# Kernel optimization log

Hardware: AMD Instinct MI355X
Metric: run time of the kernel (lower is better)

The kernel has to match this reference:

```python
import jax, jax.numpy as jnp
import numpy as np

B, T, V, D = 16, 200, 25, 128
N_Q, N_E = 4, 1024
BETA, ALPHA, SLOPE, LN_EPS = 0.25, 0.1, 0.2, 1e-5

def _ring_adjacency(v):
    A = np.zeros((v, v), dtype=np.float32)
    for i in range(v):
        A[i, (i + 1) % v] = 1.0
        A[i, (i - 1) % v] = 1.0
    A = A + np.eye(v, dtype=np.float32)  # A + I, as in module
    d_inv_sqrt = 1.0 / np.sqrt(A.sum(1))
    return (d_inv_sqrt[:, None] * A) * d_inv_sqrt[None, :]

def setup_inputs() -> dict:
    key = jax.random.key(0)
    k_z, k_e, k_w = jax.random.split(key, 3)
    z = jax.random.normal(k_z, (B, T, V, D), dtype=jnp.float32)
    # xavier_uniform for each [n_e, e_dim] codebook
    lim = float(np.sqrt(6.0 / (N_E + D)))
    emb = jax.random.uniform(k_e, (N_Q, N_E, D), dtype=jnp.float32, minval=-lim, maxval=lim)
    wlim = float(np.sqrt(1.0 / D))
    gcn_w = jax.random.uniform(k_w, (D, D), dtype=jnp.float32, minval=-wlim, maxval=wlim)
    return {
        "z": z,
        "emb": emb,
        "A_norm": jnp.asarray(_ring_adjacency(V)),
        "gcn_w": gcn_w,
        "gcn_b": jnp.zeros((D,), jnp.float32),
        "ln_scale": jnp.ones((D,), jnp.float32),
        "ln_bias": jnp.zeros((D,), jnp.float32),
    }

def _gcn_refine(residual, A_norm, gcn_w, gcn_b, ln_scale, ln_bias):
    # residual: [N, V, d]
    neigh = jnp.einsum('vw,nwd->nvd', A_norm, residual)
    neigh = neigh @ gcn_w.T + gcn_b                      # nn.Linear
    neigh = jnp.where(neigh >= 0, neigh, SLOPE * neigh)  # LeakyReLU(0.2)
    mu = neigh.mean(-1, keepdims=True)
    var = ((neigh - mu) ** 2).mean(-1, keepdims=True)
    neigh = (neigh - mu) / jnp.sqrt(var + LN_EPS) * ln_scale + ln_bias
    return residual + ALPHA * neigh

def reference(z, emb, A_norm, gcn_w, gcn_b, ln_scale, ln_bias):
    b, t, v, d = z.shape
    n_q = emb.shape[0]
    zf = z.reshape(b * t, v, d)
    residual = zf
    cum = jnp.zeros_like(zf)
    losses, idxs = [], []
    for k in range(n_q):
        refined = _gcn_refine(residual, A_norm, gcn_w, gcn_b, ln_scale, ln_bias)
        W = emb[k]                               # [n_e, d]
        flat = refined.reshape(-1, d)            # [N*V, d]
        dist = ((flat ** 2).sum(1, keepdims=True)
                - 2.0 * flat @ W.T
                + (W ** 2).sum(1)[None, :])
        idx = jnp.argmin(dist, axis=1)           # [N*V]
        q = W[idx].reshape(b * t, v, d)          # == one_hot @ W
        # commit and codebook terms are identical squared errors -> (1+beta)*mse
        diff = q - jax.lax.stop_gradient(residual)
        losses.append((1.0 + BETA) * (diff ** 2).mean(-1))
        cum = cum + q
        residual = residual - q
        idxs.append(idx.reshape(b * t, v))
    zq = zf + jax.lax.stop_gradient(cum - zf)    # straight-through
    total_loss = jnp.stack(losses, 0).mean()
    indices = jnp.stack(idxs, -1).reshape(b, t, v, n_q)
    return zq.reshape(b, t, v, d), total_loss, indices
```

## Files before the change

kernel.cpp:

```cpp
#include <hip/hip_runtime.h>

#define ZQ_N    10240000
#define IDX_OFF 10240001
#define FLT_BIG 3.402823466e38f

typedef _Float16 f16x8 __attribute__((ext_vector_type(8)));
typedef float    f32x4 __attribute__((ext_vector_type(4)));

__global__ __launch_bounds__(256) void k_wsq(const float* __restrict__ emb,
                                             float* __restrict__ wsq,
                                             float* __restrict__ loss_part) {
    int t = threadIdx.x;
    int g = blockIdx.x * 256 + t;
    if (g < 1024) loss_part[g] = 0.f;
    int row = blockIdx.x * 64 + (t >> 2);
    int seg = t & 3;
    const float4* p = (const float4*)(emb + row * 128 + seg * 32);
    float a = 0.f;
#pragma unroll
    for (int i = 0; i < 8; i++) {
        float4 w = p[i];
        a = fmaf(w.x, w.x, a); a = fmaf(w.y, w.y, a);
        a = fmaf(w.z, w.z, a); a = fmaf(w.w, w.w, a);
    }
    a += __shfl_xor(a, 1);
    a += __shfl_xor(a, 2);
    if (seg == 0) wsq[row] = a;
}

__global__ __launch_bounds__(256) void k_wsplit(const float* __restrict__ emb,
        _Float16* __restrict__ wh, _Float16* __restrict__ wl,
        const float* __restrict__ gw,
        _Float16* __restrict__ gh, _Float16* __restrict__ gl) {
    int c = blockIdx.x * 256 + threadIdx.x;
    int q   = c >> 14;
    int col = (c >> 4) & 1023;
    int k8  = (c & 15) * 8;
    const float* srcp = emb + q * 131072 + col * 128 + k8;
    float4 a = *(const float4*)(srcp);
    float4 b = *(const float4*)(srcp + 4);
    float vv[8] = {a.x, a.y, a.z, a.w, b.x, b.y, b.z, b.w};
    union { _Float16 h[8]; uint4 u4; } ph, pl;
#pragma unroll
    for (int j = 0; j < 8; j++) {
        float v = vv[j] * 1024.f;
        _Float16 h = (_Float16)v;
        float r1 = v - (float)h;
        ph.h[j] = h; pl.h[j] = (_Float16)r1;
    }
    int w  = col >> 7, p = (col >> 4) & 7, lm = col & 15;
    int ks = k8 >> 5, quad = (k8 >> 3) & 3;
    int off = ((w * 8 + p) * 4 + ks) * 512 + (quad * 16 + lm) * 8;
    *(uint4*)(wh + q * 131072 + off) = ph.u4;
    *(uint4*)(wl + q * 131072 + off) = pl.u4;

    if (c < 16384) {
        float v = gw[c] * 1024.f;
        _Float16 h = (_Float16)v;
        float r1 = v - (float)h;
        gh[c] = h; gl[c] = (_Float16)r1;
    }
}

__global__ __launch_bounds__(256) void k_refine(const float* __restrict__ zbase,
        const float* __restrict__ emb, const float* __restrict__ idx_f, int stage,
        float* __restrict__ refined, float* __restrict__ s_out,
        const float* __restrict__ An,
        const _Float16* __restrict__ gh, const _Float16* __restrict__ gl,
        const float* __restrict__ gb, const float* __restrict__ lsc,
        const float* __restrict__ lbi) {
    __shared__ __align__(16) float Rn[25 * 128];
    __shared__ __align__(16) unsigned char nbuf[2 * 32 * 136 * 2];
    __shared__ float Al[625];
    __shared__ int cds[75];
    _Float16* nh = (_Float16*)nbuf;
    _Float16* nl = (_Float16*)(nbuf + 8704);
    float*    nei = (float*)nbuf;
    const int tid = threadIdx.x;
    const int n = blockIdx.x;

    if (tid < 75) {
        int r = tid / 3, j = tid - r * 3;
        if (j < stage) cds[tid] = (int)idx_f[(n * 25 + r) * 4 + j];
    }
    for (int i = tid; i < 625; i += 256) Al[i] = An[i];
    __syncthreads();

    const float4* zp = (const float4*)(zbase + n * 3200);
    float4* Rn4 = (float4*)Rn;
    for (int i = tid; i < 800; i += 256) {
        float4 rv = zp[i];
        int r = i >> 5, c4 = (i & 31) * 4;
#pragma unroll
        for (int j = 0; j < 3; j++) {
            if (j < stage) {
                const float4 q = *(const float4*)(emb + j * 131072 + cds[r * 3 + j] * 128 + c4);
                rv.x -= q.x; rv.y -= q.y; rv.z -= q.z; rv.w -= q.w;
            }
        }
        Rn4[i] = rv;
    }
    __syncthreads();

    for (int i = tid; i < 512; i += 256) {
        int r = i >> 4, k8 = (i & 15) * 8;
        union { _Float16 h[8]; uint4 u4; } ph, pl;
        if (r < 25) {
            int vm = (r == 0) ? 24 : r - 1;
            int vp = (r == 24) ? 0 : r + 1;
            float am = Al[r * 25 + vm], a0 = Al[r * 25 + r], ap = Al[r * 25 + vp];
#pragma unroll
            for (int j = 0; j < 8; j++) {
                int d = k8 + j;
                float val = am * Rn[vm * 128 + d];
                val = fmaf(a0, Rn[r  * 128 + d], val);
                val = fmaf(ap, Rn[vp * 128 + d], val);
                float v1 = val * 1024.f;
                _Float16 h = (_Float16)v1; float fh = (float)h;
                ph.h[j] = h; pl.h[j] = (_Float16)(v1 - fh);
            }
        } else {
            ph.u4 = make_uint4(0u, 0u, 0u, 0u);
            pl.u4 = make_uint4(0u, 0u, 0u, 0u);
        }
        int off = r * 136 + k8;
        *(uint4*)(&nh[off]) = ph.u4;
        *(uint4*)(&nl[off]) = pl.u4;
    }
    __syncthreads();

    {
        const int lane = tid & 63;
        const int wv   = tid >> 6;
        const int quad = lane >> 4;
        const int lm   = lane & 15;
        const int bbase = (wv * 32 + lm) * 128 + quad * 8;
        const int abase = lm * 136 + quad * 8;

        f32x4 racc[2][2];
#pragma unroll
        for (int a = 0; a < 2; a++)
#pragma unroll
            for (int b = 0; b < 2; b++) racc[a][b] = (f32x4){0.f, 0.f, 0.f, 0.f};

#pragma unroll
        for (int k0 = 0; k0 < 4; k0++) {
            const int ko = k0 * 32;
            f16x8 ah[2], al[2];
#pragma unroll
            for (int mt = 0; mt < 2; mt++) {
                ah[mt] = *(const f16x8*)(&nh[abase + mt * (16 * 136) + ko]);
                al[mt] = *(const f16x8*)(&nl[abase + mt * (16 * 136) + ko]);
            }
            f16x8 bh[2], bl[2];
#pragma unroll
            for (int ct = 0; ct < 2; ct++) {
                bh[ct] = *(const f16x8*)(gh + bbase + ct * (16 * 128) + ko);
                bl[ct] = *(const f16x8*)(gl + bbase + ct * (16 * 128) + ko);
            }
#pragma unroll
            for (int ct = 0; ct < 2; ct++)
#pragma unroll
                for (int mt = 0; mt < 2; mt++)
                    racc[ct][mt] = __builtin_amdgcn_mfma_f32_16x16x32_f16(ah[mt], bh[ct], racc[ct][mt], 0, 0, 0);
#pragma unroll
            for (int ct = 0; ct < 2; ct++)
#pragma unroll
                for (int mt = 0; mt < 2; mt++)
                    racc[ct][mt] = __builtin_amdgcn_mfma_f32_16x16x32_f16(ah[mt], bl[ct], racc[ct][mt], 0, 0, 0);
#pragma unroll
            for (int ct = 0; ct < 2; ct++)
#pragma unroll
                for (int mt = 0; mt < 2; mt++)
                    racc[ct][mt] = __builtin_amdgcn_mfma_f32_16x16x32_f16(al[mt], bh[ct], racc[ct][mt], 0, 0, 0);
        }

        __syncthreads();

#pragma unroll
        for (int ct = 0; ct < 2; ct++)
#pragma unroll
            for (int mt = 0; mt < 2; mt++)
#pragma unroll
                for (int rg = 0; rg < 4; rg++) {
                    int row = mt * 16 + quad * 4 + rg;
                    if (row < 25)
                        nei[row * 132 + wv * 32 + ct * 16 + lm] =
                            racc[ct][mt][rg] * 9.5367431640625e-07f;
                }
    }
    __syncthreads();

    const int dpg = tid & 31;
    const int vs  = tid >> 5;
    const int dp0 = dpg * 4;

    float4 b4  = *(const float4*)(gb + dp0);
    float4 sc4 = *(const float4*)(lsc + dp0);
    float4 bi4 = *(const float4*)(lbi + dp0);
    const float bb[4] = {b4.x, b4.y, b4.z, b4.w};
    const float sc[4] = {sc4.x, sc4.y, sc4.z, sc4.w};
    const float bi[4] = {bi4.x, bi4.y, bi4.z, bi4.w};

#pragma unroll
    for (int i = 0; i < 4; i++) {
        int v = vs + 8 * i;
        if (v >= 25) break;
        float4 y4 = *(const float4*)(&nei[v * 132 + dp0]);
        const float yin[4] = {y4.x, y4.y, y4.z, y4.w};
        float y[4];
#pragma unroll
        for (int c = 0; c < 4; c++) {
            float t = yin[c] + bb[c];
            y[c] = (t >= 0.f) ? t : 0.2f * t;
        }
        float s1 = y[0] + y[1] + y[2] + y[3];
#pragma unroll
        for (int m = 1; m <= 16; m <<= 1) s1 += __shfl_xor(s1, m);
        float mu = s1 * (1.f / 128.f);
        float d2 = 0.f;
#pragma unroll
        for (int c = 0; c < 4; c++) { float t = y[c] - mu; d2 = fmaf(t, t, d2); }
#pragma unroll
        for (int m = 1; m <= 16; m <<= 1) d2 += __shfl_xor(d2, m);
        float inv = 1.f / sqrtf(d2 * (1.f / 128.f) + 1e-5f);

        float4 rn4 = *(const float4*)(&Rn[v * 128 + dp0]);
        const float rn[4] = {rn4.x, rn4.y, rn4.z, rn4.w};
        float o[4];
#pragma unroll
        for (int c = 0; c < 4; c++)
            o[c] = rn[c] + 0.1f * ((y[c] - mu) * inv * sc[c] + bi[c]);

        *(float4*)(refined + (n * 25 + v) * 128 + dp0) =
            make_float4(o[0], o[1], o[2], o[3]);

        float ss = 0.f;
#pragma unroll
        for (int c = 0; c < 4; c++) ss = fmaf(o[c], o[c], ss);
#pragma unroll
        for (int m = 1; m <= 16; m <<= 1) ss += __shfl_xor(ss, m);
        if (dpg == 0) s_out[n * 25 + v] = ss;
    }
}


#define XPAD 140

#define VQ_LOADB(BH, BL, IT) do {                                              \
    const int _o = ((w * 8 + ((IT) >> 2)) * 4 + ((IT) & 3)) * 512 + lane * 8;  \
    BH = *(const f16x8*)(wh + _o);                                             \
    BL = *(const f16x8*)(wl + _o);                                             \
} while (0)

#define VQ_STEP(IT, BH, BL) do {                                               \
    const int _ko = abase + ((IT) & 3) * 32;                                   \
    f16x8 _ah[4], _al[4];                                                      \
    _Pragma("unroll")                                                          \
    for (int _rt = 0; _rt < 4; _rt++) {                                        \
        const int _off = _ko + _rt * (16 * XPAD);                              \
        _ah[_rt] = *(const f16x8*)(&xh_s[_off]);                               \
        _al[_rt] = *(const f16x8*)(&xl_s[_off]);                               \
    }                                                                          \
    _Pragma("unroll")                                                          \
    for (int _rt = 0; _rt < 4; _rt++)                                          \
        acc[_rt] = __builtin_amdgcn_mfma_f32_16x16x32_f16(_ah[_rt], BH, acc[_rt], 0, 0, 0); \
    _Pragma("unroll")                                                          \
    for (int _rt = 0; _rt < 4; _rt++)                                          \
        acc[_rt] = __builtin_amdgcn_mfma_f32_16x16x32_f16(_ah[_rt], BL, acc[_rt], 0, 0, 0); \
    _Pragma("unroll")                                                          \
    for (int _rt = 0; _rt < 4; _rt++)                                          \
        acc[_rt] = __builtin_amdgcn_mfma_f32_16x16x32_f16(_al[_rt], BH, acc[_rt], 0, 0, 0); \
} while (0)

#define VQ_EPI(P) do {                                                         \
    float _sr[16];                                                             \
    _Pragma("unroll")                                                          \
    for (int _rt = 0; _rt < 4; _rt++) {                                        \
        float4 _t = *(const float4*)(s_g + row0 + _rt * 16 + quad * 4);        \
        _sr[_rt * 4 + 0] = _t.x; _sr[_rt * 4 + 1] = _t.y;                      \
        _sr[_rt * 4 + 2] = _t.z; _sr[_rt * 4 + 3] = _t.w;                      \
    }                                                                          \
    const int _col = w * 128 + (P) * 16 + lm;                                  \
    const float _wq = wsq_k[_col];                                             \
    _Pragma("unroll")                                                          \
    for (int _rt = 0; _rt < 4; _rt++) {                                        \
        _Pragma("unroll")                                                      \
        for (int _rg = 0; _rg < 4; _rg++) {                                    \
            float _d = (_sr[_rt * 4 + _rg]                                     \
                        - 1.9073486328125e-06f * acc[_rt][_rg]) + _wq;         \
            int _s = _rt * 4 + _rg;                                            \
            if (_d < bestv[_s]) { bestv[_s] = _d; besti[_s] = _col; }          \
        }                                                                      \
    }                                                                          \
} while (0)

__global__ __launch_bounds__(512, 1) void k_vq(const float* __restrict__ refined,
        const _Float16* __restrict__ wh,
        const _Float16* __restrict__ wl,
        const float* __restrict__ wsq_k,
        const float* __restrict__ s_g,
        float* __restrict__ idx_out, int stage) {
    __shared__ __align__(16) _Float16 xh_s[64 * XPAD];
    __shared__ __align__(16) _Float16 xl_s[64 * XPAD];
    const int tid = threadIdx.x;
    const int row0 = blockIdx.x * 64;

    const int lane = tid & 63;
    const int w    = tid >> 6;
    const int quad = lane >> 4;
    const int lm   = lane & 15;

    const int abase = lm * XPAD + quad * 8;

    f16x8 bh_a, bl_a, bh_b, bl_b;
    VQ_LOADB(bh_a, bl_a, 0);

    for (int i = tid; i < 1024; i += 512) {
        int r = i >> 4, k8 = (i & 15) * 8;
        const float* srcp = refined + (row0 + r) * 128 + k8;
        float4 a = *(const float4*)(srcp);
        float4 b = *(const float4*)(srcp + 4);
        float vv[8] = {a.x, a.y, a.z, a.w, b.x, b.y, b.z, b.w};
        union { _Float16 h[8]; uint4 u4; } ph, pl;
#pragma unroll
        for (int j = 0; j < 8; j++) {
            float v = vv[j] * 1024.f;
            _Float16 h = (_Float16)v; float fh = (float)h;
            float r1 = v - fh;
            ph.h[j] = h; pl.h[j] = (_Float16)r1;
        }
        int off = r * XPAD + k8;
        *(uint4*)(&xh_s[off]) = ph.u4;
        *(uint4*)(&xl_s[off]) = pl.u4;
    }
    __syncthreads();

    float bestv[16];
    int   besti[16];
#pragma unroll
    for (int s = 0; s < 16; s++) { bestv[s] = FLT_BIG; besti[s] = 0; }

    f32x4 acc[4];

#pragma unroll
    for (int ith = 0; ith < 16; ith++) {
        const int it0 = ith * 2, it1 = it0 + 1;
        VQ_LOADB(bh_b, bl_b, it1);
        if ((it0 & 3) == 0) {
#pragma unroll
            for (int b = 0; b < 4; b++) acc[b] = (f32x4){0.f, 0.f, 0.f, 0.f};
        }
        VQ_STEP(it0, bh_a, bl_a);
        if (it1 < 31) VQ_LOADB(bh_a, bl_a, it1 + 1);
        VQ_STEP(it1, bh_b, bl_b);
        if ((it1 & 3) == 3) VQ_EPI(it1 >> 2);
    }

#pragma unroll
    for (int s = 0; s < 16; s++) {
#pragma unroll
        for (int m = 1; m <= 8; m <<= 1) {
            float ov = __shfl_xor(bestv[s], m);
            int   oi = __shfl_xor(besti[s], m);
            if (ov < bestv[s] || (ov == bestv[s] && oi < besti[s])) {
                bestv[s] = ov; besti[s] = oi;
            }
        }
    }

    __syncthreads();
    float* redv = (float*)xh_s;
    int*   redi = (int*)xl_s;
    if (lm == 0) {
#pragma unroll
        for (int s = 0; s < 16; s++) {
            int row = (s >> 2) * 16 + quad * 4 + (s & 3);
            redv[w * 64 + row] = bestv[s];
            redi[w * 64 + row] = besti[s];
        }
    }
    __syncthreads();
    if (tid < 64) {
        float bv = redv[tid]; int bi = redi[tid];
#pragma unroll
        for (int ww = 1; ww < 8; ww++) {
            float v2 = redv[ww * 64 + tid]; int i2 = redi[ww * 64 + tid];
            if (v2 < bv || (v2 == bv && i2 < bi)) { bv = v2; bi = i2; }
        }
        idx_out[(row0 + tid) * 4 + stage] = (float)bi;
    }
}

#define FIN_STAGE(K, ACC) do {                                                 \
    const float4 q = *(const float4*)(emb + (K) * 131072 + codes[r * 4 + (K)] * 128 + c4); \
    float dx = q.x - rv.x, dy = q.y - rv.y, dz = q.z - rv.z, dw = q.w - rv.w;  \
    ACC = fmaf(dx, dx, ACC); ACC = fmaf(dy, dy, ACC);                          \
    ACC = fmaf(dz, dz, ACC); ACC = fmaf(dw, dw, ACC);                          \
    s4.x += q.x; s4.y += q.y; s4.z += q.z; s4.w += q.w;                        \
    rv.x -= q.x; rv.y -= q.y; rv.z -= q.z; rv.w -= q.w;                        \
} while (0)

__global__ __launch_bounds__(256) void k_final(const float* __restrict__ z,
        const float* __restrict__ emb, const float* __restrict__ idx_f,
        float* __restrict__ zq, float* __restrict__ loss_part) {
    __shared__ int codes[256];
    const int tid = threadIdx.x;
    const int row0 = blockIdx.x * 64;
    codes[tid] = (int)idx_f[row0 * 4 + tid];
    __syncthreads();

    const float4* zp = (const float4*)(z + row0 * 128);
    float4* zqp = (float4*)(zq + row0 * 128);
    float a0 = 0.f, a1 = 0.f, a2 = 0.f, a3 = 0.f;
#pragma unroll
    for (int j = 0; j < 8; j++) {
        int idx4 = tid + j * 256;
        int r = idx4 >> 5;
        int c4 = (idx4 & 31) * 4;
        float4 rv = zp[idx4];
        float4 s4 = make_float4(0.f, 0.f, 0.f, 0.f);
        FIN_STAGE(0, a0);
        FIN_STAGE(1, a1);
        FIN_STAGE(2, a2);
        FIN_STAGE(3, a3);
        zqp[idx4] = s4;
    }
#pragma unroll
    for (int m = 1; m <= 32; m <<= 1) {
        a0 += __shfl_xor(a0, m); a1 += __shfl_xor(a1, m);
        a2 += __shfl_xor(a2, m); a3 += __shfl_xor(a3, m);
    }
    if ((tid & 63) == 0) {
        float* slot = &loss_part[blockIdx.x & 1023];
        atomicAdd(slot, a0); atomicAdd(slot, a1);
        atomicAdd(slot, a2); atomicAdd(slot, a3);
    }
}

__global__ __launch_bounds__(256) void k_loss(const float* __restrict__ loss_part,
                                              float* __restrict__ out) {
    int t = threadIdx.x;
    float a = loss_part[t] + loss_part[t + 256] + loss_part[t + 512] + loss_part[t + 768];
#pragma unroll
    for (int m = 1; m <= 32; m <<= 1) a += __shfl_xor(a, m);
    __shared__ float w[4];
    if ((t & 63) == 0) w[t >> 6] = a;
    __syncthreads();
    if (t == 0) {
        float s = w[0] + w[1] + w[2] + w[3];
        out[ZQ_N] = s * (1.25f / (128.f * 320000.f));
    }
}

extern "C" void kernel_launch(void* const* d_in, const int* in_sizes, int n_in,
                              void* d_out, int out_size, void* d_ws, size_t ws_size,
                              hipStream_t stream) {
    (void)in_sizes; (void)n_in; (void)out_size; (void)ws_size;
    const float* z   = (const float*)d_in[0];
    const float* emb = (const float*)d_in[1];
    const float* An  = (const float*)d_in[2];
    const float* gw  = (const float*)d_in[3];
    const float* gb  = (const float*)d_in[4];
    const float* lsc = (const float*)d_in[5];
    const float* lbi = (const float*)d_in[6];

    float* out     = (float*)d_out;
    float* zq      = out;
    float* idx_out = out + IDX_OFF;

    float* ws        = (float*)d_ws;
    float* refined   = ws + 10240000;
    _Float16* gh_f16 = (_Float16*)(ws + 20480000);
    _Float16* gl_f16 = (_Float16*)(ws + 20488192);
    _Float16* wh_f16 = (_Float16*)(ws + 20496384);
    _Float16* wl_f16 = (_Float16*)(ws + 20758528);
    float* s_g       = ws + 21020672;
    float* wsq       = ws + 21100672;
    float* loss_part = ws + 21104768;

    k_wsq<<<64, 256, 0, stream>>>(emb, wsq, loss_part);
    k_wsplit<<<256, 256, 0, stream>>>(emb, wh_f16, wl_f16, gw, gh_f16, gl_f16);
    for (int k = 0; k < 4; k++) {
        k_refine<<<3200, 256, 0, stream>>>(z, emb, idx_out, k,
                                           refined, s_g, An,
                                           gh_f16, gl_f16, gb, lsc, lbi);
        k_vq<<<1250, 512, 0, stream>>>(refined,
                                       wh_f16 + k * 131072, wl_f16 + k * 131072,
                                       wsq + k * 1024,
                                       s_g, idx_out, k);
    }
    k_final<<<1250, 256, 0, stream>>>(z, emb, idx_out, zq, loss_part);
    k_loss<<<1, 256, 0, stream>>>(loss_part, out);
}
```

Before: 722.3 us.

## Reorder VQ MFMA loop to reuse A fragments across four codebook column tiles

The VQ distance kernel used to reload the A (activation hi/lo fp16) fragments from LDS at every k-step for each 16-column codebook tile. It now keeps four accumulator sets (acc[4][4]) and loops k-outer, column-tile-inner, so each A fragment load serves four column tiles. This cuts LDS reads by about four times. The argmin epilogue now runs twice, over groups of four tiles. The cost is a much larger accumulator register footprint (64 floats), which may raise VGPR/AGPR pressure or cause spills.

```diff
diff --git a/kernel.cpp b/kernel.cpp
--- a/kernel.cpp
+++ b/kernel.cpp
@@ -247,33 +247,48 @@
 
 #define XPAD 140
 
-#define VQ_LOADB(BH, BL, IT) do {                                              \
-    const int _o = ((w * 8 + ((IT) >> 2)) * 4 + ((IT) & 3)) * 512 + lane * 8;  \
+#define VQ_LOADA(KS) do {                                                      \
+    _Pragma("unroll")                                                          \
+    for (int _rt = 0; _rt < 4; _rt++) {                                        \
+        const int _off = abase + _rt * (16 * XPAD) + (KS) * 32;                \
+        ah[_rt] = *(const f16x8*)(&xh_s[_off]);                                \
+        al[_rt] = *(const f16x8*)(&xl_s[_off]);                                \
+    }                                                                          \
+} while (0)
+
+#define VQ_LOADB(BH, BL, P, KS) do {                                           \
+    const int _o = ((w * 8 + (P)) * 4 + (KS)) * 512 + lane * 8;                \
     BH = *(const f16x8*)(wh + _o);                                             \
     BL = *(const f16x8*)(wl + _o);                                             \
 } while (0)
 
-#define VQ_STEP(IT, BH, BL) do {                                               \
-    const int _ko = abase + ((IT) & 3) * 32;                                   \
-    f16x8 _ah[4], _al[4];                                                      \
-    _Pragma("unroll")                                                          \
-    for (int _rt = 0; _rt < 4; _rt++) {                                        \
-        const int _off = _ko + _rt * (16 * XPAD);                              \
-        _ah[_rt] = *(const f16x8*)(&xh_s[_off]);                               \
-        _al[_rt] = *(const f16x8*)(&xl_s[_off]);                               \
-    }                                                                          \
+#define VQ_MMA(PI, BH, BL) do {                                                \
     _Pragma("unroll")                                                          \
     for (int _rt = 0; _rt < 4; _rt++)                                          \
-        acc[_rt] = __builtin_amdgcn_mfma_f32_16x16x32_f16(_ah[_rt], BH, acc[_rt], 0, 0, 0); \
+        acc[PI][_rt] = __builtin_amdgcn_mfma_f32_16x16x32_f16(ah[_rt], BH, acc[PI][_rt], 0, 0, 0); \
     _Pragma("unroll")                                                          \
     for (int _rt = 0; _rt < 4; _rt++)                                          \
-        acc[_rt] = __builtin_amdgcn_mfma_f32_16x16x32_f16(_ah[_rt], BL, acc[_rt], 0, 0, 0); \
+        acc[PI][_rt] = __builtin_amdgcn_mfma_f32_16x16x32_f16(ah[_rt], BL, acc[PI][_rt], 0, 0, 0); \
     _Pragma("unroll")                                                          \
     for (int _rt = 0; _rt < 4; _rt++)                                          \
-        acc[_rt] = __builtin_amdgcn_mfma_f32_16x16x32_f16(_al[_rt], BH, acc[_rt], 0, 0, 0); \
-} while (0)
-
-#define VQ_EPI(P) do {                                                         \
+        acc[PI][_rt] = __builtin_amdgcn_mfma_f32_16x16x32_f16(al[_rt], BH, acc[PI][_rt], 0, 0, 0); \
+} while (0)
+
+#define VQ_ZERO do {                                                           \
+    _Pragma("unroll")                                                          \
+    for (int _a = 0; _a < 4; _a++)                                             \
+        _Pragma("unroll")                                                      \
+        for (int _b = 0; _b < 4; _b++) acc[_a][_b] = (f32x4){0.f, 0.f, 0.f, 0.f}; \
+} while (0)
+
+#define PIPE(G, IT, CH, CL, NH, NL) do {                                       \
+    if ((IT) < 15) VQ_LOADB(NH, NL, (G) * 4 + (((IT) + 1) & 3), ((IT) + 1) >> 2); \
+    else if ((G) == 0) VQ_LOADB(NH, NL, 4, 0);                                 \
+    if (((IT) & 3) == 0) VQ_LOADA((IT) >> 2);                                  \
+    VQ_MMA((IT) & 3, CH, CL);                                                  \
+} while (0)
+
+#define VQ_EPI(G) do {                                                         \
     float _sr[16];                                                             \
     _Pragma("unroll")                                                          \
     for (int _rt = 0; _rt < 4; _rt++) {                                        \
@@ -281,16 +296,19 @@
         _sr[_rt * 4 + 0] = _t.x; _sr[_rt * 4 + 1] = _t.y;                      \
         _sr[_rt * 4 + 2] = _t.z; _sr[_rt * 4 + 3] = _t.w;                      \
     }                                                                          \
-    const int _col = w * 128 + (P) * 16 + lm;                                  \
-    const float _wq = wsq_k[_col];                                             \
-    _Pragma("unroll")                                                          \
-    for (int _rt = 0; _rt < 4; _rt++) {                                        \
+    _Pragma("unroll")                                                          \
+    for (int _pi = 0; _pi < 4; _pi++) {                                        \
+        const int _col = w * 128 + ((G) * 4 + _pi) * 16 + lm;                  \
+        const float _wq = wsq_k[_col];                                         \
         _Pragma("unroll")                                                      \
-        for (int _rg = 0; _rg < 4; _rg++) {                                    \
-            float _d = (_sr[_rt * 4 + _rg]                                     \
-                        - 1.9073486328125e-06f * acc[_rt][_rg]) + _wq;         \
-            int _s = _rt * 4 + _rg;                                            \
-            if (_d < bestv[_s]) { bestv[_s] = _d; besti[_s] = _col; }          \
+        for (int _rt = 0; _rt < 4; _rt++) {                                    \
+            _Pragma("unroll")                                                  \
+            for (int _rg = 0; _rg < 4; _rg++) {                                \
+                float _d = (_sr[_rt * 4 + _rg]                                 \
+                            - 1.9073486328125e-06f * acc[_pi][_rt][_rg]) + _wq;\
+                int _s = _rt * 4 + _rg;                                        \
+                if (_d < bestv[_s]) { bestv[_s] = _d; besti[_s] = _col; }      \
+            }                                                                  \
         }                                                                      \
     }                                                                          \
 } while (0)
@@ -313,8 +331,9 @@
 
     const int abase = lm * XPAD + quad * 8;
 
-    f16x8 bh_a, bl_a, bh_b, bl_b;
-    VQ_LOADB(bh_a, bl_a, 0);
+    f16x8 ah[4], al[4];
+    f16x8 b0h, b0l, b1h, b1l;
+    VQ_LOADB(b0h, b0l, 0, 0);
 
     for (int i = tid; i < 1024; i += 512) {
         int r = i >> 4, k8 = (i & 15) * 8;
@@ -341,21 +360,45 @@
 #pragma unroll
     for (int s = 0; s < 16; s++) { bestv[s] = FLT_BIG; besti[s] = 0; }
 
-    f32x4 acc[4];
-
-#pragma unroll
-    for (int ith = 0; ith < 16; ith++) {
-        const int it0 = ith * 2, it1 = it0 + 1;
-        VQ_LOADB(bh_b, bl_b, it1);
-        if ((it0 & 3) == 0) {
-#pragma unroll
-            for (int b = 0; b < 4; b++) acc[b] = (f32x4){0.f, 0.f, 0.f, 0.f};
-        }
-        VQ_STEP(it0, bh_a, bl_a);
-        if (it1 < 31) VQ_LOADB(bh_a, bl_a, it1 + 1);
-        VQ_STEP(it1, bh_b, bl_b);
-        if ((it1 & 3) == 3) VQ_EPI(it1 >> 2);
-    }
+    f32x4 acc[4][4];
+
+    VQ_ZERO;
+    PIPE(0, 0,  b0h, b0l, b1h, b1l);
+    PIPE(0, 1,  b1h, b1l, b0h, b0l);
+    PIPE(0, 2,  b0h, b0l, b1h, b1l);
+    PIPE(0, 3,  b1h, b1l, b0h, b0l);
+    PIPE(0, 4,  b0h, b0l, b1h, b1l);
+    PIPE(0, 5,  b1h, b1l, b0h, b0l);
+    PIPE(0, 6,  b0h, b0l, b1h, b1l);
+    PIPE(0, 7,  b1h, b1l, b0h, b0l);
+    PIPE(0, 8,  b0h, b0l, b1h, b1l);
+    PIPE(0, 9,  b1h, b1l, b0h, b0l);
+    PIPE(0, 10, b0h, b0l, b1h, b1l);
+    PIPE(0, 11, b1h, b1l, b0h, b0l);
+    PIPE(0, 12, b0h, b0l, b1h, b1l);
+    PIPE(0, 13, b1h, b1l, b0h, b0l);
+    PIPE(0, 14, b0h, b0l, b1h, b1l);
+    PIPE(0, 15, b1h, b1l, b0h, b0l);
+    VQ_EPI(0);
+
+    VQ_ZERO;
+    PIPE(1, 0,  b0h, b0l, b1h, b1l);
+    PIPE(1, 1,  b1h, b1l, b0h, b0l);
+    PIPE(1, 2,  b0h, b0l, b1h, b1l);
+    PIPE(1, 3,  b1h, b1l, b0h, b0l);
+    PIPE(1, 4,  b0h, b0l, b1h, b1l);
+    PIPE(1, 5,  b1h, b1l, b0h, b0l);
+    PIPE(1, 6,  b0h, b0l, b1h, b1l);
+    PIPE(1, 7,  b1h, b1l, b0h, b0l);
+    PIPE(1, 8,  b0h, b0l, b1h, b1l);
+    PIPE(1, 9,  b1h, b1l, b0h, b0l);
+    PIPE(1, 10, b0h, b0l, b1h, b1l);
+    PIPE(1, 11, b1h, b1l, b0h, b0l);
+    PIPE(1, 12, b0h, b0l, b1h, b1l);
+    PIPE(1, 13, b1h, b1l, b0h, b0l);
+    PIPE(1, 14, b0h, b0l, b1h, b1l);
+    PIPE(1, 15, b1h, b1l, b0h, b0l);
+    VQ_EPI(1);
 
 #pragma unroll
     for (int s = 0; s < 16; s++) {
```

New measurement: 725.8 us. About the same (+0.5%).
